# Performance work log

Measured on AMD Instinct MI355X. Metric: run time of the kernel, lower is better.

Reference implementation:

```python
import jax, jax.numpy as jnp
import numpy as np

B, Q, C, K = 2, 300, 80, 300
MH = MW = 128
TH = TW = 320


def setup_inputs() -> dict:
    key = jax.random.key(0)
    k1, k2, k3 = jax.random.split(key, 3)
    pred_logits = jax.random.normal(k1, (B, Q, C), dtype=jnp.float32)
    pred_boxes = jax.random.uniform(k2, (B, Q, 4), dtype=jnp.float32)  # cxcywh in [0,1]
    pred_masks = jax.random.normal(k3, (B, Q, MH, MW), dtype=jnp.float32)
    # fixed target size so resize output shape is static (original uses .item() per image)
    orig_target_sizes = jnp.full((B, 2), 320.0, dtype=jnp.float32)  # (w, h)
    return {
        'pred_logits': pred_logits,
        'pred_boxes': pred_boxes,
        'pred_masks': pred_masks,
        'orig_target_sizes': orig_target_sizes,
        'target_h': TH,
        'target_w': TW,
    }


def reference(pred_logits, pred_boxes, pred_masks, orig_target_sizes, target_h, target_w):
    b, q, c = pred_logits.shape
    # cxcywh -> xyxy
    cx, cy, w, h = jnp.split(pred_boxes, 4, axis=-1)
    boxes_xyxy = jnp.concatenate([cx - 0.5 * w, cy - 0.5 * h, cx + 0.5 * w, cy + 0.5 * h], axis=-1)
    # scale factor [w, h, w, h] per image
    scale_fct = jnp.concatenate([orig_target_sizes, orig_target_sizes], axis=1)[:, None, :]  # [B,1,4]
    boxes_abs = boxes_xyxy * scale_fct  # [B,Q,4]

    # focal-loss path: sigmoid scores, topk over flattened (query, class)
    scores_flat = jax.nn.sigmoid(pred_logits).reshape(b, q * c)
    scores, index_flat = jax.lax.top_k(scores_flat, K)  # [B,K]
    labels = index_flat % c
    query_indices = index_flat // c  # [B,K]

    top_boxes = jnp.take_along_axis(boxes_abs, query_indices[:, :, None], axis=1)  # [B,K,4]
    top_masks = jnp.take_along_axis(pred_masks, query_indices[:, :, None, None], axis=1)  # [B,K,MH,MW]

    # bilinear resize, half-pixel centers == torch align_corners=False
    resized = jax.image.resize(top_masks, (b, K, target_h, target_w), method='linear')
    binary_masks = (jax.nn.sigmoid(resized) > 0.5).astype(jnp.float32)

    return scores, labels, top_boxes, binary_masks
```

## Files before the change

### kernel.cpp

```cpp
#include <hip/hip_runtime.h>
#include <stdint.h>

constexpr int Bq = 2;
constexpr int Qn = 300;
constexpr int Cn = 80;
constexpr int Kn = 300;
constexpr int NFLAT = Qn * Cn;
constexpr int MHs = 128;
constexpr int MWs = 128;
constexpr int THs = 320;
constexpr int TWs = 320;

constexpr int OFF_SCORES = 0;
constexpr int OFF_LABELS = Bq * Kn;
constexpr int OFF_BOXES  = 2 * Bq * Kn;
constexpr int OFF_MASKS  = 2 * Bq * Kn + Bq * Kn * 4;

constexpr int TPB = 1024;
constexpr int EPT = (NFLAT + TPB - 1) / TPB;

typedef float vf4 __attribute__((ext_vector_type(4)));

__global__ __launch_bounds__(TPB) void topk_kernel(
    const float* __restrict__ logits,
    const float* __restrict__ boxes,
    const float* __restrict__ osz,
    float* __restrict__ out,
    int* __restrict__ qidx_ws)
{
    const int b   = blockIdx.x;
    const int tid = threadIdx.x;
    const float* lg = logits + (size_t)b * NFLAT;

    uint32_t bits[EPT];
    #pragma unroll
    for (int j = 0; j < EPT; ++j) {
        int idx = j * TPB + tid;
        bool valid = (idx < NFLAT);
        float x = valid ? lg[idx] : 0.0f;
        float s = 1.0f / (1.0f + expf(-x));
        bits[j] = valid ? __float_as_uint(s) : 0u;
    }

    __shared__ uint32_t bins[8192];
    __shared__ int scanA[1024], scanB[1024];
    __shared__ unsigned long long sk[1024];
    __shared__ int s_cnt, s_seg, s_B;

    {
        uint4* b4 = (uint4*)bins;
        for (int i = tid; i < 8192 / 4; i += TPB) b4[i] = make_uint4(0, 0, 0, 0);
    }
    if (tid == 0) s_cnt = 0;
    __syncthreads();

    #pragma unroll
    for (int j = 0; j < EPT; ++j) {
        int idx = j * TPB + tid;
        if (idx < NFLAT) {
            uint32_t bin = bits[j] >> 18;
            atomicAdd(&bins[bin >> 1], 1u << ((bin & 1u) * 16));
        }
    }
    __syncthreads();

    int sum = 0;
    #pragma unroll
    for (int k = 0; k < 8; ++k) {
        uint32_t v = bins[tid * 8 + k];
        sum += (int)(v & 0xFFFFu) + (int)(v >> 16);
    }
    scanA[tid] = sum;
    __syncthreads();

    int* src = scanA;
    int* dst = scanB;
    for (int d = 1; d < 1024; d <<= 1) {
        int v = src[tid] + ((tid + d < 1024) ? src[tid + d] : 0);
        dst[tid] = v;
        __syncthreads();
        int* t = src; src = dst; dst = t;
    }

    int sfx  = src[tid];
    int sfx1 = (tid < 1023) ? src[tid + 1] : 0;
    if (sfx >= Kn && sfx1 < Kn) s_seg = tid;
    __syncthreads();

    if (tid == 0) {
        int t = s_seg;
        int cumAbove = (t < 1023) ? src[t + 1] : 0;
        int B = t * 16;
        for (int i = 15; i >= 0; --i) {
            int bin = t * 16 + i;
            int c = (int)((bins[bin >> 1] >> ((bin & 1) * 16)) & 0xFFFFu);
            if (cumAbove + c >= Kn) { B = bin; break; }
            cumAbove += c;
        }
        s_B = B;
    }
    __syncthreads();

    const uint32_t Bv = (uint32_t)s_B;
    #pragma unroll
    for (int j = 0; j < EPT; ++j) {
        int idx = j * TPB + tid;
        if (idx < NFLAT && (bits[j] >> 18) >= Bv) {
            int p = atomicAdd(&s_cnt, 1);
            if (p < 1024) {
                sk[p] = ((uint64_t)bits[j] << 32)
                      | (uint64_t)(0xFFFFFFFFu - (uint32_t)idx);
            }
        }
    }
    __syncthreads();

    const int n = min(s_cnt, 1024);
    if (tid < n) {
        unsigned long long my = sk[tid];
        int rank = 0;
        for (int i = 0; i < n; ++i) rank += (sk[i] > my);
        if (rank < Kn) {
            uint32_t idx = 0xFFFFFFFFu - (uint32_t)(my & 0xFFFFFFFFull);
            float score  = __uint_as_float((uint32_t)(my >> 32));
            int label = (int)(idx % (uint32_t)Cn);
            int q     = (int)(idx / (uint32_t)Cn);

            out[OFF_SCORES + b * Kn + rank] = score;
            out[OFF_LABELS + b * Kn + rank] = (float)label;

            const float sw = osz[b * 2 + 0];
            const float sh = osz[b * 2 + 1];
            const float* bx = boxes + ((size_t)(b * Qn + q)) * 4;
            float cx = bx[0], cy = bx[1], w = bx[2], h = bx[3];
            float* ob = out + OFF_BOXES + ((size_t)(b * Kn + rank)) * 4;
            ob[0] = (cx - 0.5f * w) * sw;
            ob[1] = (cy - 0.5f * h) * sh;
            ob[2] = (cx + 0.5f * w) * sw;
            ob[3] = (cy + 0.5f * h) * sh;

            qidx_ws[b * Kn + rank] = q;
        }
    }
}

__global__ __launch_bounds__(320) void resize_kernel(
    const float* __restrict__ masks,
    const int* __restrict__ qidx_ws,
    float* __restrict__ out)
{
    const int blk = blockIdx.x;
    const int bk  = blk >> 2;
    const int s   = blk & 3;
    const int tid = threadIdx.x;
    const int b   = bk / Kn;
    const int q   = qidx_ws[bk];

    const int qm = tid % 80;
    const int rb = tid / 80;

    const float* M = masks + ((size_t)(b * Qn + q)) * (MHs * MWs);

    float wxa[4], wxb[4];
    int   c0[4], c1[4];
    #pragma unroll
    for (int t = 0; t < 4; ++t) {
        int ox = 4 * qm + t;
        float sx = fmaf(0.4f, (float)ox, -0.3f);
        int ix0 = (int)floorf(sx);
        float fr = sx - (float)ix0;
        wxb[t] = fr;
        wxa[t] = 1.0f - fr;
        c0[t] = max(ix0, 0);
        c1[t] = min(ix0 + 1, MWs - 1);
    }

    #define HROW(dst, r)                                                    \
        {                                                                   \
            const float* row_ = M + (r) * MWs;                              \
            _Pragma("unroll")                                               \
            for (int t = 0; t < 4; ++t)                                     \
                dst[t] = fmaf(wxa[t], row_[c0[t]], wxb[t] * row_[c1[t]]);   \
        }

    const int Y0 = 80 * s + 20 * rb;
    const int M0 = Y0 / 5;

    float h0[4], h1[4], h2[4], h3[4];
    HROW(h2, max(2 * M0 - 1, 0));
    HROW(h3, 2 * M0);

    float* outm = out + OFF_MASKS + (size_t)bk * (THs * TWs);

    #pragma unroll
    for (int g = 0; g < 4; ++g) {
        #pragma unroll
        for (int t = 0; t < 4; ++t) { h0[t] = h2[t]; h1[t] = h3[t]; }
        const int Mg = M0 + g;
        HROW(h2, 2 * Mg + 1);
        HROW(h3, min(2 * Mg + 2, MHs - 1));

        float* rp = outm + (size_t)(Y0 + 5 * g) * TWs + 4 * qm;
        vf4 o;

        #define EMIT(wA, hA, wB, hB, rowoff)                                 \
            {                                                                \
                _Pragma("unroll")                                            \
                for (int t = 0; t < 4; ++t) {                                \
                    float v = fmaf(wA, hA[t], (wB) * hB[t]);                 \
                    o[t] = (v > 0.0f) ? 1.0f : 0.0f;                         \
                }                                                            \
                __builtin_nontemporal_store(o, (vf4*)(rp + (rowoff) * TWs)); \
            }

        EMIT(0.3f, h0, 0.7f, h1, 0)
        EMIT(0.9f, h1, 0.1f, h2, 1)
        EMIT(0.5f, h1, 0.5f, h2, 2)
        EMIT(0.1f, h1, 0.9f, h2, 3)
        EMIT(0.7f, h2, 0.3f, h3, 4)

        #undef EMIT
    }
    #undef HROW
}

extern "C" void kernel_launch(void* const* d_in, const int* in_sizes, int n_in,
                              void* d_out, int out_size, void* d_ws, size_t ws_size,
                              hipStream_t stream) {
    const float* logits = (const float*)d_in[0];
    const float* boxes  = (const float*)d_in[1];
    const float* masks  = (const float*)d_in[2];
    const float* osz    = (const float*)d_in[3];

    float* out = (float*)d_out;
    int* qidx  = (int*)d_ws;

    topk_kernel<<<Bq, TPB, 0, stream>>>(logits, boxes, osz, out, qidx);
    resize_kernel<<<Bq * Kn * 4, 320, 0, stream>>>(masks, qidx, out);
}
```

Before: 344.3 us.

## Bitonic sort for top-k and restructure resize to vectorized 8-column tiles

```diff
diff --git a/kernel.cpp b/kernel.cpp
--- a/kernel.cpp
+++ b/kernel.cpp
@@ -51,6 +51,7 @@
         uint4* b4 = (uint4*)bins;
         for (int i = tid; i < 8192 / 4; i += TPB) b4[i] = make_uint4(0, 0, 0, 0);
     }
+    sk[tid] = 0ull;
     if (tid == 0) s_cnt = 0;
     __syncthreads();
 
@@ -115,113 +116,114 @@
     }
     __syncthreads();
 
-    const int n = min(s_cnt, 1024);
-    if (tid < n) {
+    for (int k2 = 2; k2 <= 1024; k2 <<= 1) {
+        for (int j = k2 >> 1; j > 0; j >>= 1) {
+            int ixj = tid ^ j;
+            if (ixj > tid) {
+                unsigned long long a = sk[tid], c2 = sk[ixj];
+                bool up = ((tid & k2) == 0);
+                if (up ? (a < c2) : (a > c2)) { sk[tid] = c2; sk[ixj] = a; }
+            }
+            __syncthreads();
+        }
+    }
+
+    if (tid < Kn) {
         unsigned long long my = sk[tid];
-        int rank = 0;
-        for (int i = 0; i < n; ++i) rank += (sk[i] > my);
-        if (rank < Kn) {
-            uint32_t idx = 0xFFFFFFFFu - (uint32_t)(my & 0xFFFFFFFFull);
-            float score  = __uint_as_float((uint32_t)(my >> 32));
-            int label = (int)(idx % (uint32_t)Cn);
-            int q     = (int)(idx / (uint32_t)Cn);
-
-            out[OFF_SCORES + b * Kn + rank] = score;
-            out[OFF_LABELS + b * Kn + rank] = (float)label;
-
-            const float sw = osz[b * 2 + 0];
-            const float sh = osz[b * 2 + 1];
-            const float* bx = boxes + ((size_t)(b * Qn + q)) * 4;
-            float cx = bx[0], cy = bx[1], w = bx[2], h = bx[3];
-            float* ob = out + OFF_BOXES + ((size_t)(b * Kn + rank)) * 4;
-            ob[0] = (cx - 0.5f * w) * sw;
-            ob[1] = (cy - 0.5f * h) * sh;
-            ob[2] = (cx + 0.5f * w) * sw;
-            ob[3] = (cy + 0.5f * h) * sh;
-
-            qidx_ws[b * Kn + rank] = q;
-        }
+        uint32_t idx = 0xFFFFFFFFu - (uint32_t)(my & 0xFFFFFFFFull);
+        float score  = __uint_as_float((uint32_t)(my >> 32));
+        int label = (int)(idx % (uint32_t)Cn);
+        int q     = (int)(idx / (uint32_t)Cn);
+
+        out[OFF_SCORES + b * Kn + tid] = score;
+        out[OFF_LABELS + b * Kn + tid] = (float)label;
+
+        const float sw = osz[b * 2 + 0];
+        const float sh = osz[b * 2 + 1];
+        const float* bx = boxes + ((size_t)(b * Qn + q)) * 4;
+        float cx = bx[0], cy = bx[1], w = bx[2], h = bx[3];
+        float* ob = out + OFF_BOXES + ((size_t)(b * Kn + tid)) * 4;
+        ob[0] = (cx - 0.5f * w) * sw;
+        ob[1] = (cy - 0.5f * h) * sh;
+        ob[2] = (cx + 0.5f * w) * sw;
+        ob[3] = (cy + 0.5f * h) * sh;
+
+        qidx_ws[b * Kn + tid] = q;
     }
 }
 
-__global__ __launch_bounds__(320) void resize_kernel(
+__global__ __launch_bounds__(256) void resize_kernel(
     const float* __restrict__ masks,
     const int* __restrict__ qidx_ws,
     float* __restrict__ out)
 {
     const int blk = blockIdx.x;
-    const int bk  = blk >> 2;
-    const int s   = blk & 3;
+    const int bk  = blk >> 1;
+    const int hh  = blk & 1;
     const int tid = threadIdx.x;
     const int b   = bk / Kn;
     const int q   = qidx_ws[bk];
-
-    const int qm = tid % 80;
-    const int rb = tid / 80;
+    const int c   = tid & 15;
+    const int s   = tid >> 4;
 
     const float* M = masks + ((size_t)(b * Qn + q)) * (MHs * MWs);
-
-    float wxa[4], wxb[4];
-    int   c0[4], c1[4];
-    #pragma unroll
-    for (int t = 0; t < 4; ++t) {
-        int ox = 4 * qm + t;
-        float sx = fmaf(0.4f, (float)ox, -0.3f);
-        int ix0 = (int)floorf(sx);
-        float fr = sx - (float)ix0;
-        wxb[t] = fr;
-        wxa[t] = 1.0f - fr;
-        c0[t] = max(ix0, 0);
-        c1[t] = min(ix0 + 1, MWs - 1);
-    }
-
-    #define HROW(dst, r)                                                    \
-        {                                                                   \
-            const float* row_ = M + (r) * MWs;                              \
-            _Pragma("unroll")                                               \
-            for (int t = 0; t < 4; ++t)                                     \
-                dst[t] = fmaf(wxa[t], row_[c0[t]], wxb[t] * row_[c1[t]]);   \
-        }
-
-    const int Y0 = 80 * s + 20 * rb;
-    const int M0 = Y0 / 5;
-
-    float h0[4], h1[4], h2[4], h3[4];
-    HROW(h2, max(2 * M0 - 1, 0));
-    HROW(h3, 2 * M0);
+    const int colm1 = max(8 * c - 1, 0);
+    const int colp8 = min(8 * c + 8, MWs - 1);
+
+    float hA[20], hB[20], hC[20], hD[20];
+
+    auto hrow = [&](float* hv, int r) {
+        const float* row = M + r * MWs;
+        vf4 u0 = *(const vf4*)(row + 8 * c);
+        vf4 u1 = *(const vf4*)(row + 8 * c + 4);
+        float a[10];
+        a[0] = row[colm1];
+        a[1] = u0[0]; a[2] = u0[1]; a[3] = u0[2]; a[4] = u0[3];
+        a[5] = u1[0]; a[6] = u1[1]; a[7] = u1[2]; a[8] = u1[3];
+        a[9] = row[colp8];
+        #pragma unroll
+        for (int u = 0; u < 4; ++u) {
+            hv[5*u+0] = 0.3f * a[2*u]   + 0.7f * a[2*u+1];
+            hv[5*u+1] = 0.9f * a[2*u+1] + 0.1f * a[2*u+2];
+            hv[5*u+2] = 0.5f * a[2*u+1] + 0.5f * a[2*u+2];
+            hv[5*u+3] = 0.1f * a[2*u+1] + 0.9f * a[2*u+2];
+            hv[5*u+4] = 0.7f * a[2*u+2] + 0.3f * a[2*u+3];
+        }
+    };
 
     float* outm = out + OFF_MASKS + (size_t)bk * (THs * TWs);
-
-    #pragma unroll
-    for (int g = 0; g < 4; ++g) {
+    auto emit5 = [&](int row, float wA, const float* pA, float wB, const float* pB) {
+        float* rp = outm + (size_t)row * TWs + 20 * c;
         #pragma unroll
-        for (int t = 0; t < 4; ++t) { h0[t] = h2[t]; h1[t] = h3[t]; }
-        const int Mg = M0 + g;
-        HROW(h2, 2 * Mg + 1);
-        HROW(h3, min(2 * Mg + 2, MHs - 1));
-
-        float* rp = outm + (size_t)(Y0 + 5 * g) * TWs + 4 * qm;
-        vf4 o;
-
-        #define EMIT(wA, hA, wB, hB, rowoff)                                 \
-            {                                                                \
-                _Pragma("unroll")                                            \
-                for (int t = 0; t < 4; ++t) {                                \
-                    float v = fmaf(wA, hA[t], (wB) * hB[t]);                 \
-                    o[t] = (v > 0.0f) ? 1.0f : 0.0f;                         \
-                }                                                            \
-                __builtin_nontemporal_store(o, (vf4*)(rp + (rowoff) * TWs)); \
+        for (int v = 0; v < 5; ++v) {
+            vf4 o;
+            #pragma unroll
+            for (int t = 0; t < 4; ++t) {
+                float val = fmaf(wA, pA[4*v+t], wB * pB[4*v+t]);
+                o[t] = (val > 0.0f) ? 1.0f : 0.0f;
             }
-
-        EMIT(0.3f, h0, 0.7f, h1, 0)
-        EMIT(0.9f, h1, 0.1f, h2, 1)
-        EMIT(0.5f, h1, 0.5f, h2, 2)
-        EMIT(0.1f, h1, 0.9f, h2, 3)
-        EMIT(0.7f, h2, 0.3f, h3, 4)
-
-        #undef EMIT
-    }
-    #undef HROW
+            __builtin_nontemporal_store(o, (vf4*)(rp + 4 * v));
+        }
+    };
+
+    const int Mb = 32 * hh + 2 * s;
+    const int Y0 = 160 * hh + 10 * s;
+    hrow(hA, max(2 * Mb - 1, 0));
+    hrow(hB, 2 * Mb);
+    #pragma unroll
+    for (int g = 0; g < 2; ++g) {
+        const int Mg = Mb + g;
+        hrow(hC, 2 * Mg + 1);
+        hrow(hD, min(2 * Mg + 2, MHs - 1));
+        const int Y = Y0 + 5 * g;
+        emit5(Y + 0, 0.3f, hA, 0.7f, hB);
+        emit5(Y + 1, 0.9f, hB, 0.1f, hC);
+        emit5(Y + 2, 0.5f, hB, 0.5f, hC);
+        emit5(Y + 3, 0.1f, hB, 0.9f, hC);
+        emit5(Y + 4, 0.7f, hC, 0.3f, hD);
+        #pragma unroll
+        for (int i = 0; i < 20; ++i) { hA[i] = hC[i]; hB[i] = hD[i]; }
+    }
 }
 
 extern "C" void kernel_launch(void* const* d_in, const int* in_sizes, int n_in,
@@ -236,5 +238,5 @@
     int* qidx  = (int*)d_ws;
 
     topk_kernel<<<Bq, TPB, 0, stream>>>(logits, boxes, osz, out, qidx);
-    resize_kernel<<<Bq * Kn * 4, 320, 0, stream>>>(masks, qidx, out);
+    resize_kernel<<<Bq * Kn * 2, 256, 0, stream>>>(masks, qidx, out);
 }
```

New measurement: 801.5 us. 133% more time.

## Replace histogram top-k threshold with bisection search; vectorize mask row gathers

Applied to the files above, without the earlier changes.

```diff
diff --git a/kernel.cpp b/kernel.cpp
--- a/kernel.cpp
+++ b/kernel.cpp
@@ -19,7 +19,8 @@
 constexpr int TPB = 1024;
 constexpr int EPT = (NFLAT + TPB - 1) / TPB;
 
-typedef float vf4 __attribute__((ext_vector_type(4)));
+typedef float vf4  __attribute__((ext_vector_type(4)));
+typedef float uvf4 __attribute__((ext_vector_type(4), aligned(4)));
 
 __global__ __launch_bounds__(TPB) void topk_kernel(
     const float* __restrict__ logits,
@@ -32,94 +33,61 @@
     const int tid = threadIdx.x;
     const float* lg = logits + (size_t)b * NFLAT;
 
-    uint32_t bits[EPT];
+    uint32_t key[EPT];
     #pragma unroll
     for (int j = 0; j < EPT; ++j) {
         int idx = j * TPB + tid;
         bool valid = (idx < NFLAT);
         float x = valid ? lg[idx] : 0.0f;
         float s = 1.0f / (1.0f + expf(-x));
-        bits[j] = valid ? __float_as_uint(s) : 0u;
-    }
-
-    __shared__ uint32_t bins[8192];
-    __shared__ int scanA[1024], scanB[1024];
+        key[j] = valid ? __float_as_uint(s) : 0u;
+    }
+
+    __shared__ uint32_t sh_lo, sh_hi;
+    __shared__ int sh_cnt, sh_done;
     __shared__ unsigned long long sk[1024];
-    __shared__ int s_cnt, s_seg, s_B;
-
-    {
-        uint4* b4 = (uint4*)bins;
-        for (int i = tid; i < 8192 / 4; i += TPB) b4[i] = make_uint4(0, 0, 0, 0);
-    }
-    if (tid == 0) s_cnt = 0;
+
+    if (tid == 0) { sh_lo = 0u; sh_hi = 0xFFFFFFFFu; sh_cnt = 0; sh_done = 0; }
     __syncthreads();
 
+    for (int it = 0; it < 32; ++it) {
+        if (sh_done) break;
+        uint32_t lo = sh_lo, hi = sh_hi;
+        if (hi - lo <= 1) break;
+        uint32_t mid = lo + ((hi - lo) >> 1);
+        int c = 0;
+        #pragma unroll
+        for (int j = 0; j < EPT; ++j) c += (key[j] > mid) ? 1 : 0;
+        for (int off = 32; off > 0; off >>= 1) c += __shfl_down(c, off);
+        if ((tid & 63) == 0 && c) atomicAdd(&sh_cnt, c);
+        __syncthreads();
+        if (tid == 0) {
+            int total = sh_cnt;
+            sh_cnt = 0;
+            if (total >= Kn) { sh_lo = mid; if (total <= 768) sh_done = 1; }
+            else             { sh_hi = mid; }
+        }
+        __syncthreads();
+    }
+
+    const uint32_t T = sh_lo;
     #pragma unroll
     for (int j = 0; j < EPT; ++j) {
         int idx = j * TPB + tid;
-        if (idx < NFLAT) {
-            uint32_t bin = bits[j] >> 18;
-            atomicAdd(&bins[bin >> 1], 1u << ((bin & 1u) * 16));
+        if (idx < NFLAT && key[j] > T) {
+            int p = atomicAdd(&sh_cnt, 1);
+            if (p < 1024)
+                sk[p] = ((unsigned long long)key[j] << 32)
+                      | (unsigned long long)(0xFFFFFFFFu - (uint32_t)idx);
         }
     }
     __syncthreads();
 
-    int sum = 0;
-    #pragma unroll
-    for (int k = 0; k < 8; ++k) {
-        uint32_t v = bins[tid * 8 + k];
-        sum += (int)(v & 0xFFFFu) + (int)(v >> 16);
-    }
-    scanA[tid] = sum;
-    __syncthreads();
-
-    int* src = scanA;
-    int* dst = scanB;
-    for (int d = 1; d < 1024; d <<= 1) {
-        int v = src[tid] + ((tid + d < 1024) ? src[tid + d] : 0);
-        dst[tid] = v;
-        __syncthreads();
-        int* t = src; src = dst; dst = t;
-    }
-
-    int sfx  = src[tid];
-    int sfx1 = (tid < 1023) ? src[tid + 1] : 0;
-    if (sfx >= Kn && sfx1 < Kn) s_seg = tid;
-    __syncthreads();
-
-    if (tid == 0) {
-        int t = s_seg;
-        int cumAbove = (t < 1023) ? src[t + 1] : 0;
-        int B = t * 16;
-        for (int i = 15; i >= 0; --i) {
-            int bin = t * 16 + i;
-            int c = (int)((bins[bin >> 1] >> ((bin & 1) * 16)) & 0xFFFFu);
-            if (cumAbove + c >= Kn) { B = bin; break; }
-            cumAbove += c;
-        }
-        s_B = B;
-    }
-    __syncthreads();
-
-    const uint32_t Bv = (uint32_t)s_B;
-    #pragma unroll
-    for (int j = 0; j < EPT; ++j) {
-        int idx = j * TPB + tid;
-        if (idx < NFLAT && (bits[j] >> 18) >= Bv) {
-            int p = atomicAdd(&s_cnt, 1);
-            if (p < 1024) {
-                sk[p] = ((uint64_t)bits[j] << 32)
-                      | (uint64_t)(0xFFFFFFFFu - (uint32_t)idx);
-            }
-        }
-    }
-    __syncthreads();
-
-    const int n = min(s_cnt, 1024);
+    const int n = min(sh_cnt, 1024);
     if (tid < n) {
         unsigned long long my = sk[tid];
         int rank = 0;
-        for (int i = 0; i < n; ++i) rank += (sk[i] > my);
+        for (int i = 0; i < n; ++i) rank += (sk[i] > my) ? 1 : 0;
         if (rank < Kn) {
             uint32_t idx = 0xFFFFFFFFu - (uint32_t)(my & 0xFFFFFFFFull);
             float score  = __uint_as_float((uint32_t)(my >> 32));
@@ -155,73 +123,78 @@
     const int tid = threadIdx.x;
     const int b   = bk / Kn;
     const int q   = qidx_ws[bk];
-
-    const int qm = tid % 80;
-    const int rb = tid / 80;
+    const int c   = tid % 80;
+    const int rs  = tid / 80;
 
     const float* M = masks + ((size_t)(b * Qn + q)) * (MHs * MWs);
 
-    float wxa[4], wxb[4];
-    int   c0[4], c1[4];
+    int s0;
+    {
+        float sx0 = fmaf(0.4f, (float)(4 * c), -0.3f);
+        int i0 = (int)floorf(sx0);
+        s0 = min(max(i0, 0), MWs - 4);
+    }
+    float W[4][4];
     #pragma unroll
     for (int t = 0; t < 4; ++t) {
-        int ox = 4 * qm + t;
+        int ox = 4 * c + t;
         float sx = fmaf(0.4f, (float)ox, -0.3f);
         int ix0 = (int)floorf(sx);
         float fr = sx - (float)ix0;
-        wxb[t] = fr;
-        wxa[t] = 1.0f - fr;
-        c0[t] = max(ix0, 0);
-        c1[t] = min(ix0 + 1, MWs - 1);
-    }
-
-    #define HROW(dst, r)                                                    \
-        {                                                                   \
-            const float* row_ = M + (r) * MWs;                              \
-            _Pragma("unroll")                                               \
-            for (int t = 0; t < 4; ++t)                                     \
-                dst[t] = fmaf(wxa[t], row_[c0[t]], wxb[t] * row_[c1[t]]);   \
-        }
-
-    const int Y0 = 80 * s + 20 * rb;
+        int ca = max(ix0, 0);
+        int cb = min(ix0 + 1, MWs - 1);
+        float wa = 1.0f - fr, wb = fr;
+        #pragma unroll
+        for (int j = 0; j < 4; ++j) {
+            float w = 0.0f;
+            if (s0 + j == ca) w += wa;
+            if (s0 + j == cb) w += wb;
+            W[t][j] = w;
+        }
+    }
+
+    auto hrow = [&](float* hv, int r) {
+        uvf4 a = *(const uvf4*)(M + r * MWs + s0);
+        #pragma unroll
+        for (int t = 0; t < 4; ++t)
+            hv[t] = fmaf(W[t][0], a[0],
+                    fmaf(W[t][1], a[1],
+                    fmaf(W[t][2], a[2], W[t][3] * a[3])));
+    };
+
+    float* outm = out + OFF_MASKS + (size_t)bk * (THs * TWs);
+    auto emit = [&](int row, float wA, const float* pA, float wB, const float* pB) {
+        vf4 o;
+        #pragma unroll
+        for (int t = 0; t < 4; ++t) {
+            float v = fmaf(wA, pA[t], wB * pB[t]);
+            o[t] = (v > 0.0f) ? 1.0f : 0.0f;
+        }
+        __builtin_nontemporal_store(o, (vf4*)(outm + (size_t)row * TWs + 4 * c));
+    };
+
+    const int Y0 = 80 * s + 20 * rs;
     const int M0 = Y0 / 5;
 
-    float h0[4], h1[4], h2[4], h3[4];
-    HROW(h2, max(2 * M0 - 1, 0));
-    HROW(h3, 2 * M0);
-
-    float* outm = out + OFF_MASKS + (size_t)bk * (THs * TWs);
+    float hA[4], hB[4], hC[4], hD[4];
+    hrow(hC, max(2 * M0 - 1, 0));
+    hrow(hD, 2 * M0);
 
     #pragma unroll
     for (int g = 0; g < 4; ++g) {
         #pragma unroll
-        for (int t = 0; t < 4; ++t) { h0[t] = h2[t]; h1[t] = h3[t]; }
+        for (int t = 0; t < 4; ++t) { hA[t] = hC[t]; hB[t] = hD[t]; }
         const int Mg = M0 + g;
-        HROW(h2, 2 * Mg + 1);
-        HROW(h3, min(2 * Mg + 2, MHs - 1));
-
-        float* rp = outm + (size_t)(Y0 + 5 * g) * TWs + 4 * qm;
-        vf4 o;
-
-        #define EMIT(wA, hA, wB, hB, rowoff)                                 \
-            {                                                                \
-                _Pragma("unroll")                                            \
-                for (int t = 0; t < 4; ++t) {                                \
-                    float v = fmaf(wA, hA[t], (wB) * hB[t]);                 \
-                    o[t] = (v > 0.0f) ? 1.0f : 0.0f;                         \
-                }                                                            \
-                __builtin_nontemporal_store(o, (vf4*)(rp + (rowoff) * TWs)); \
-            }
-
-        EMIT(0.3f, h0, 0.7f, h1, 0)
-        EMIT(0.9f, h1, 0.1f, h2, 1)
-        EMIT(0.5f, h1, 0.5f, h2, 2)
-        EMIT(0.1f, h1, 0.9f, h2, 3)
-        EMIT(0.7f, h2, 0.3f, h3, 4)
-
-        #undef EMIT
-    }
-    #undef HROW
+        hrow(hC, 2 * Mg + 1);
+        hrow(hD, min(2 * Mg + 2, MHs - 1));
+
+        const int Y = Y0 + 5 * g;
+        emit(Y + 0, 0.3f, hA, 0.7f, hB);
+        emit(Y + 1, 0.9f, hB, 0.1f, hC);
+        emit(Y + 2, 0.5f, hB, 0.5f, hC);
+        emit(Y + 3, 0.1f, hB, 0.9f, hC);
+        emit(Y + 4, 0.7f, hC, 0.3f, hD);
+    }
 }
 
 extern "C" void kernel_launch(void* const* d_in, const int* in_sizes, int n_in,
```

Measured after the change: 331.4 us. -3.8%, faster.
